# Kernel tuning notes

Measured on AMD Instinct MI355X. Metric: run time of the kernel, lower is better.

## Reference

```python
import jax, jax.numpy as jnp
import numpy as np

NUM_MOE = 64
DIM = 64


def setup_inputs() -> dict:
    key = jax.random.key(0)
    k1, k2 = jax.random.split(key)
    x = jax.random.normal(k1, (32, 8192, DIM), dtype=jnp.float32)
    # nn.Linear(dim, num_moe, bias=False): weight shape [num_moe, dim]
    W = jax.random.normal(k2, (NUM_MOE, DIM), dtype=jnp.float32) * (1.0 / np.sqrt(DIM))
    return {"x": x, "W": W, "topk": 2}


def reference(x, W, topk):
    # logits = x @ W.T  -> [B, S, E]
    logits = jnp.einsum("bsd,ed->bse", x, W)
    probs = jax.nn.softmax(logits, axis=-1)
    # top-k selection over experts
    _, topk_idx = jax.lax.top_k(probs, topk)  # [B, S, k]
    # scatter: keep top-k probs, fill rest with -inf. Since the scattered
    # values are exactly probs at those indices, a mask + where is identical
    # to full_like(-inf).scatter_(idx, vals).
    mask = jnp.sum(jax.nn.one_hot(topk_idx, NUM_MOE, dtype=jnp.bool_), axis=-2) > 0  # [B,S,E]
    topk_probs = jnp.where(mask, probs, -jnp.inf)
    # renormalize with a second softmax (non-selected experts -> 0)
    return jax.nn.softmax(topk_probs, axis=-1)
```

## Files before the change

### kernel.cpp

```cpp
#include <hip/hip_runtime.h>
#include <math.h>

#define NUM_MOE 64
#define DIM 64
#define CH 16
#define TOK 64
#define NW 4
#define ET 8

typedef float f32x2 __attribute__((ext_vector_type(2)));
typedef float f32x4 __attribute__((ext_vector_type(4)));
typedef float f32x8 __attribute__((ext_vector_type(8)));

__global__ __launch_bounds__(256)
void moe_router_kernel(const float* __restrict__ x,
                       const float* __restrict__ W,
                       float* __restrict__ out,
                       int ntok) {
    __shared__ f32x4 xs[TOK * CH];
    __shared__ float pm1[NW][TOK], pm2[NW][TOK], pz[NW][TOK];
    __shared__ int   pi1[NW][TOK], pi2[NW][TOK];

    const int tid    = threadIdx.x;
    const long tbase = (long)blockIdx.x * TOK;

    {
        const f32x4* __restrict__ g4 = reinterpret_cast<const f32x4*>(x) + tbase * CH;
        #pragma unroll
        for (int j = 0; j < 4; ++j) {
            const int G  = tid + j * 256;
            const int tk = G >> 4;
            const int c  = G & 15;
            const int Gc = (tbase + tk < ntok) ? G : (G & 15);
            xs[tk * CH + (c ^ (tk & 7))] = g4[Gc];
        }
    }

    {
        f32x4* __restrict__ ob = reinterpret_cast<f32x4*>(out) + tbase * CH;
        const f32x4 z4 = {0.0f, 0.0f, 0.0f, 0.0f};
        #pragma unroll
        for (int j = 0; j < 4; ++j) {
            const int F = tid + j * 256;
            if (tbase + (F >> 4) < ntok) ob[F] = z4;
        }
    }
    __syncthreads();

    const int lane = tid & 63;
    const int wid  = __builtin_amdgcn_readfirstlane(tid >> 6);
    const f32x8* __restrict__ Wg8 =
        reinterpret_cast<const f32x8*>(W) + (size_t)wid * 16 * (DIM / 8);

    float m1 = -INFINITY, m2 = -INFINITY, Zp = 0.0f;
    int   i1 = 0, i2 = 0;

    #pragma unroll
    for (int p = 0; p < 2; ++p) {
        f32x2 acc[ET];
        #pragma unroll
        for (int e = 0; e < ET; ++e) acc[e] = (f32x2){0.0f, 0.0f};

        #pragma unroll
        for (int k8 = 0; k8 < 8; ++k8) {
            const f32x4 xk0 = xs[lane * CH + ((2 * k8) ^ (lane & 7))];
            const f32x4 xk1 = xs[lane * CH + ((2 * k8 + 1) ^ (lane & 7))];
            const f32x2 xa = {xk0.x, xk0.y};
            const f32x2 xb = {xk0.z, xk0.w};
            const f32x2 xc = {xk1.x, xk1.y};
            const f32x2 xd = {xk1.z, xk1.w};
            #pragma unroll
            for (int e = 0; e < ET; ++e) {
                const f32x8 w8 = Wg8[(p * ET + e) * (DIM / 8) + k8];
                const f32x2 wa = {w8[0], w8[1]};
                const f32x2 wb = {w8[2], w8[3]};
                const f32x2 wc = {w8[4], w8[5]};
                const f32x2 wd = {w8[6], w8[7]};
                acc[e] = __builtin_elementwise_fma(xa, wa, acc[e]);
                acc[e] = __builtin_elementwise_fma(xb, wb, acc[e]);
                acc[e] = __builtin_elementwise_fma(xc, wc, acc[e]);
                acc[e] = __builtin_elementwise_fma(xd, wd, acc[e]);
            }
        }
        #pragma unroll
        for (int e = 0; e < ET; ++e) {
            const float v  = acc[e].x + acc[e].y;
            const int   ge = wid * 16 + p * ET + e;
            Zp += __expf(v);
            const bool b1 = v > m1;
            const bool b2 = v > m2;
            i2 = b1 ? i1 : (b2 ? ge : i2);
            m2 = b1 ? m1 : (b2 ? v : m2);
            i1 = b1 ? ge : i1;
            m1 = b1 ? v  : m1;
        }
    }

    pm1[wid][lane] = m1;  pm2[wid][lane] = m2;  pz[wid][lane] = Zp;
    pi1[wid][lane] = i1;  pi2[wid][lane] = i2;
    __syncthreads();

    if (tid < 64) {
        const int tk = tid;
        float M1 = pm1[0][tk], M2 = pm2[0][tk], Z = pz[0][tk];
        int   I1 = pi1[0][tk], I2 = pi2[0][tk];
        #pragma unroll
        for (int w = 1; w < NW; ++w) {
            const float b1 = pm1[w][tk], b2 = pm2[w][tk];
            const int   j1 = pi1[w][tk], j2 = pi2[w][tk];
            Z += pz[w][tk];
            const bool rep = b1 > M1;
            const float nm2 = rep ? ((b2 > M1) ? b2 : M1) : ((b1 > M2) ? b1 : M2);
            const int   ni2 = rep ? ((b2 > M1) ? j2 : I1) : ((b1 > M2) ? j1 : I2);
            M1 = rep ? b1 : M1;
            I1 = rep ? j1 : I1;
            M2 = nm2;  I2 = ni2;
        }

        const float E1  = __expf(M1), E2 = __expf(M2);
        const float d12 = (E1 - E2) / Z;
        const float w1  = 1.0f / (1.0f + __expf(-d12));
        const float w2  = 1.0f - w1;

        if (tbase + tk < ntok) {
            float* __restrict__ orow = out + (tbase + tk) * DIM;
            orow[I1] = w1;
            orow[I2] = w2;
        }
    }
}

extern "C" void kernel_launch(void* const* d_in, const int* in_sizes, int n_in,
                              void* d_out, int out_size, void* d_ws, size_t ws_size,
                              hipStream_t stream) {
    const float* x = (const float*)d_in[0];
    const float* W = (const float*)d_in[1];
    float* out = (float*)d_out;
    int ntok = in_sizes[0] / DIM;

    int blocks = (ntok + TOK - 1) / TOK;
    moe_router_kernel<<<blocks, 256, 0, stream>>>(x, W, out, ntok);
}
```

Before: 42.22 us.

## Process four token tiles per block with double-buffered register prefetch

Each block now loops over four 64-token tiles, loading the next tile's x into registers while computing the current one, then storing it to a second shared-memory buffer. The final top-2 reduction is rotated across waves, and the partial results are packed into fewer shared arrays. The aim is to hide global load latency and amortise per-block setup. The trade-off is fewer blocks, less occupancy-based latency hiding, and zero-fill stores that are all issued and waited on up front.

```diff
diff --git a/kernel.cpp b/kernel.cpp
--- a/kernel.cpp
+++ b/kernel.cpp
@@ -7,6 +7,7 @@
 #define TOK 64
 #define NW 4
 #define ET 8
+#define NT 4
 
 typedef float f32x2 __attribute__((ext_vector_type(2)));
 typedef float f32x4 __attribute__((ext_vector_type(4)));
@@ -17,115 +18,148 @@
                        const float* __restrict__ W,
                        float* __restrict__ out,
                        int ntok) {
-    __shared__ f32x4 xs[TOK * CH];
-    __shared__ float pm1[NW][TOK], pm2[NW][TOK], pz[NW][TOK];
-    __shared__ int   pi1[NW][TOK], pi2[NW][TOK];
-
-    const int tid    = threadIdx.x;
-    const long tbase = (long)blockIdx.x * TOK;
-
-    {
-        const f32x4* __restrict__ g4 = reinterpret_cast<const f32x4*>(x) + tbase * CH;
-        #pragma unroll
-        for (int j = 0; j < 4; ++j) {
-            const int G  = tid + j * 256;
-            const int tk = G >> 4;
-            const int c  = G & 15;
-            const int Gc = (tbase + tk < ntok) ? G : (G & 15);
-            xs[tk * CH + (c ^ (tk & 7))] = g4[Gc];
-        }
-    }
-
-    {
-        f32x4* __restrict__ ob = reinterpret_cast<f32x4*>(out) + tbase * CH;
-        const f32x4 z4 = {0.0f, 0.0f, 0.0f, 0.0f};
-        #pragma unroll
-        for (int j = 0; j < 4; ++j) {
-            const int F = tid + j * 256;
-            if (tbase + (F >> 4) < ntok) ob[F] = z4;
-        }
-    }
-    __syncthreads();
-
+    __shared__ f32x4 xs[2][TOK * CH];
+    __shared__ f32x2 pmm[2][NW][TOK];
+    __shared__ float pzz[2][NW][TOK];
+    __shared__ int   pii[2][NW][TOK];
+    const int tid  = threadIdx.x;
     const int lane = tid & 63;
     const int wid  = __builtin_amdgcn_readfirstlane(tid >> 6);
+    const long tile0 = (long)blockIdx.x * NT;
+
+    const f32x4* __restrict__ g4 = reinterpret_cast<const f32x4*>(x);
     const f32x8* __restrict__ Wg8 =
         reinterpret_cast<const f32x8*>(W) + (size_t)wid * 16 * (DIM / 8);
 
-    float m1 = -INFINITY, m2 = -INFINITY, Zp = 0.0f;
-    int   i1 = 0, i2 = 0;
+    f32x4 st[4];
+    {
+        const long tb = tile0 * TOK;
+        #pragma unroll
+        for (int j = 0; j < 4; ++j) {
+            const int G = tid + j * 256;
+            const long tk = tb + (G >> 4);
+            st[j] = g4[(tk < ntok) ? (tb * CH + G) : 0];
+        }
+    }
+    {
+        f32x4* __restrict__ ob = reinterpret_cast<f32x4*>(out) + tile0 * TOK * CH;
+        const f32x4 z4 = {0.0f, 0.0f, 0.0f, 0.0f};
+        #pragma unroll
+        for (int jj = 0; jj < 4 * NT; ++jj) {
+            const int F = tid + jj * 256;
+            if (tile0 * TOK + (F >> 4) < ntok) ob[F] = z4;
+        }
+    }
+    #pragma unroll
+    for (int j = 0; j < 4; ++j) {
+        const int G  = tid + j * 256;
+        const int tk = G >> 4, c = G & 15;
+        xs[0][tk * CH + (c ^ (tk & 7))] = st[j];
+    }
+    asm volatile("s_waitcnt vmcnt(0)" ::: "memory");
+    __syncthreads();
 
-    #pragma unroll
-    for (int p = 0; p < 2; ++p) {
-        f32x2 acc[ET];
-        #pragma unroll
-        for (int e = 0; e < ET; ++e) acc[e] = (f32x2){0.0f, 0.0f};
+    for (int it = 0; it < NT; ++it) {
+        const int  c  = it & 1;
+        const long tb = (tile0 + it) * TOK;
+        const bool have_next = (it + 1 < NT);
+
+        if (have_next) {
+            const long tbn = (tile0 + it + 1) * TOK;
+            #pragma unroll
+            for (int j = 0; j < 4; ++j) {
+                const int G = tid + j * 256;
+                const long tk = tbn + (G >> 4);
+                st[j] = g4[(tk < ntok) ? (tbn * CH + G) : 0];
+            }
+        }
+
+        float m1 = -INFINITY, m2 = -INFINITY, Zp = 0.0f;
+        int   i1 = 0, i2 = 0;
 
         #pragma unroll
-        for (int k8 = 0; k8 < 8; ++k8) {
-            const f32x4 xk0 = xs[lane * CH + ((2 * k8) ^ (lane & 7))];
-            const f32x4 xk1 = xs[lane * CH + ((2 * k8 + 1) ^ (lane & 7))];
-            const f32x2 xa = {xk0.x, xk0.y};
-            const f32x2 xb = {xk0.z, xk0.w};
-            const f32x2 xc = {xk1.x, xk1.y};
-            const f32x2 xd = {xk1.z, xk1.w};
+        for (int p = 0; p < 2; ++p) {
+            f32x2 acc[ET];
+            #pragma unroll
+            for (int e = 0; e < ET; ++e) acc[e] = (f32x2){0.0f, 0.0f};
+
+            #pragma unroll
+            for (int k8 = 0; k8 < 8; ++k8) {
+                const f32x4 xk0 = xs[c][lane * CH + ((2 * k8) ^ (lane & 7))];
+                const f32x4 xk1 = xs[c][lane * CH + ((2 * k8 + 1) ^ (lane & 7))];
+                const f32x2 xa = {xk0.x, xk0.y};
+                const f32x2 xb = {xk0.z, xk0.w};
+                const f32x2 xc = {xk1.x, xk1.y};
+                const f32x2 xd = {xk1.z, xk1.w};
+                #pragma unroll
+                for (int e = 0; e < ET; ++e) {
+                    const f32x8 w8 = Wg8[(p * ET + e) * (DIM / 8) + k8];
+                    const f32x2 wa = {w8[0], w8[1]};
+                    const f32x2 wb = {w8[2], w8[3]};
+                    const f32x2 wc = {w8[4], w8[5]};
+                    const f32x2 wd = {w8[6], w8[7]};
+                    acc[e] = __builtin_elementwise_fma(xa, wa, acc[e]);
+                    acc[e] = __builtin_elementwise_fma(xb, wb, acc[e]);
+                    acc[e] = __builtin_elementwise_fma(xc, wc, acc[e]);
+                    acc[e] = __builtin_elementwise_fma(xd, wd, acc[e]);
+                }
+            }
+            if (p == 0 && have_next) {
+                #pragma unroll
+                for (int j = 0; j < 4; ++j) {
+                    const int G  = tid + j * 256;
+                    const int tk = G >> 4, cc = G & 15;
+                    xs[c ^ 1][tk * CH + (cc ^ (tk & 7))] = st[j];
+                }
+            }
             #pragma unroll
             for (int e = 0; e < ET; ++e) {
-                const f32x8 w8 = Wg8[(p * ET + e) * (DIM / 8) + k8];
-                const f32x2 wa = {w8[0], w8[1]};
-                const f32x2 wb = {w8[2], w8[3]};
-                const f32x2 wc = {w8[4], w8[5]};
-                const f32x2 wd = {w8[6], w8[7]};
-                acc[e] = __builtin_elementwise_fma(xa, wa, acc[e]);
-                acc[e] = __builtin_elementwise_fma(xb, wb, acc[e]);
-                acc[e] = __builtin_elementwise_fma(xc, wc, acc[e]);
-                acc[e] = __builtin_elementwise_fma(xd, wd, acc[e]);
+                const float v  = acc[e].x + acc[e].y;
+                const int   ge = wid * 16 + p * ET + e;
+                Zp += __expf(v);
+                const bool b1 = v > m1;
+                const bool b2 = v > m2;
+                i2 = b1 ? i1 : (b2 ? ge : i2);
+                m2 = b1 ? m1 : (b2 ? v : m2);
+                i1 = b1 ? ge : i1;
+                m1 = b1 ? v  : m1;
             }
         }
-        #pragma unroll
-        for (int e = 0; e < ET; ++e) {
-            const float v  = acc[e].x + acc[e].y;
-            const int   ge = wid * 16 + p * ET + e;
-            Zp += __expf(v);
-            const bool b1 = v > m1;
-            const bool b2 = v > m2;
-            i2 = b1 ? i1 : (b2 ? ge : i2);
-            m2 = b1 ? m1 : (b2 ? v : m2);
-            i1 = b1 ? ge : i1;
-            m1 = b1 ? v  : m1;
-        }
-    }
 
-    pm1[wid][lane] = m1;  pm2[wid][lane] = m2;  pz[wid][lane] = Zp;
-    pi1[wid][lane] = i1;  pi2[wid][lane] = i2;
-    __syncthreads();
+        pmm[c][wid][lane] = (f32x2){m1, m2};
+        pzz[c][wid][lane] = Zp;
+        pii[c][wid][lane] = i1 | (i2 << 8);
+        __syncthreads();
 
-    if (tid < 64) {
-        const int tk = tid;
-        float M1 = pm1[0][tk], M2 = pm2[0][tk], Z = pz[0][tk];
-        int   I1 = pi1[0][tk], I2 = pi2[0][tk];
-        #pragma unroll
-        for (int w = 1; w < NW; ++w) {
-            const float b1 = pm1[w][tk], b2 = pm2[w][tk];
-            const int   j1 = pi1[w][tk], j2 = pi2[w][tk];
-            Z += pz[w][tk];
-            const bool rep = b1 > M1;
-            const float nm2 = rep ? ((b2 > M1) ? b2 : M1) : ((b1 > M2) ? b1 : M2);
-            const int   ni2 = rep ? ((b2 > M1) ? j2 : I1) : ((b1 > M2) ? j1 : I2);
-            M1 = rep ? b1 : M1;
-            I1 = rep ? j1 : I1;
-            M2 = nm2;  I2 = ni2;
-        }
-
-        const float E1  = __expf(M1), E2 = __expf(M2);
-        const float d12 = (E1 - E2) / Z;
-        const float w1  = 1.0f / (1.0f + __expf(-d12));
-        const float w2  = 1.0f - w1;
-
-        if (tbase + tk < ntok) {
-            float* __restrict__ orow = out + (tbase + tk) * DIM;
-            orow[I1] = w1;
-            orow[I2] = w2;
+        if (wid == (it & (NW - 1))) {
+            const int tk = lane;
+            f32x2 mm0 = pmm[c][0][tk];
+            float M1 = mm0.x, M2 = mm0.y, Z = pzz[c][0][tk];
+            int   pk0 = pii[c][0][tk];
+            int   I1 = pk0 & 0xFF, I2 = pk0 >> 8;
+            #pragma unroll
+            for (int w = 1; w < NW; ++w) {
+                const f32x2 mmw = pmm[c][w][tk];
+                const float b1 = mmw.x, b2 = mmw.y;
+                const int   pkw = pii[c][w][tk];
+                const int   j1 = pkw & 0xFF, j2 = pkw >> 8;
+                Z += pzz[c][w][tk];
+                const bool rep = b1 > M1;
+                const float nm2 = rep ? ((b2 > M1) ? b2 : M1) : ((b1 > M2) ? b1 : M2);
+                const int   ni2 = rep ? ((b2 > M1) ? j2 : I1) : ((b1 > M2) ? j1 : I2);
+                M1 = rep ? b1 : M1;
+                I1 = rep ? j1 : I1;
+                M2 = nm2;  I2 = ni2;
+            }
+            const float E1  = __expf(M1), E2 = __expf(M2);
+            const float d12 = (E1 - E2) / Z;
+            const float w1  = 1.0f / (1.0f + __expf(-d12));
+            const float w2  = 1.0f - w1;
+            if (tb + tk < ntok) {
+                float* __restrict__ orow = out + (tb + tk) * DIM;
+                orow[I1] = w1;
+                orow[I2] = w2;
+            }
         }
     }
 }
@@ -138,6 +172,7 @@
     float* out = (float*)d_out;
     int ntok = in_sizes[0] / DIM;
 
-    int blocks = (ntok + TOK - 1) / TOK;
+    int tiles  = (ntok + TOK - 1) / TOK;
+    int blocks = (tiles + NT - 1) / NT;
     moe_router_kernel<<<blocks, 256, 0, stream>>>(x, W, out, ntok);
 }
```

After: 89.64 us. 112% more time.

## Process two tokens per lane with 128-token tiles to reuse weight loads

Applied to the files above, without the earlier changes.

Doubles the tokens per block from 64 to 128 and has each lane compute logits for two tokens, so each W vector load feeds twice as many FMAs. The shared-memory partial results are packed, with the two maxima in an f32x2 and the two indices in one int. The aim is to cut weight-load and per-block overhead per token. In exchange it raises register pressure and LDS use, and halves the block count, which may reduce occupancy and latency hiding.

```diff
diff --git a/kernel.cpp b/kernel.cpp
--- a/kernel.cpp
+++ b/kernel.cpp
@@ -4,7 +4,7 @@
 #define NUM_MOE 64
 #define DIM 64
 #define CH 16
-#define TOK 64
+#define TOK 128
 #define NW 4
 #define ET 8
 
@@ -18,16 +18,16 @@
                        float* __restrict__ out,
                        int ntok) {
     __shared__ f32x4 xs[TOK * CH];
-    __shared__ float pm1[NW][TOK], pm2[NW][TOK], pz[NW][TOK];
-    __shared__ int   pi1[NW][TOK], pi2[NW][TOK];
-
+    __shared__ f32x2 pmm[NW][TOK];
+    __shared__ float pzz[NW][TOK];
+    __shared__ int   pii[NW][TOK];
     const int tid    = threadIdx.x;
     const long tbase = (long)blockIdx.x * TOK;
 
     {
         const f32x4* __restrict__ g4 = reinterpret_cast<const f32x4*>(x) + tbase * CH;
         #pragma unroll
-        for (int j = 0; j < 4; ++j) {
+        for (int j = 0; j < 8; ++j) {
             const int G  = tid + j * 256;
             const int tk = G >> 4;
             const int c  = G & 15;
@@ -35,12 +35,11 @@
             xs[tk * CH + (c ^ (tk & 7))] = g4[Gc];
         }
     }
-
     {
         f32x4* __restrict__ ob = reinterpret_cast<f32x4*>(out) + tbase * CH;
         const f32x4 z4 = {0.0f, 0.0f, 0.0f, 0.0f};
         #pragma unroll
-        for (int j = 0; j < 4; ++j) {
+        for (int j = 0; j < 8; ++j) {
             const int F = tid + j * 256;
             if (tbase + (F >> 4) < ntok) ob[F] = z4;
         }
@@ -52,23 +51,30 @@
     const f32x8* __restrict__ Wg8 =
         reinterpret_cast<const f32x8*>(W) + (size_t)wid * 16 * (DIM / 8);
 
-    float m1 = -INFINITY, m2 = -INFINITY, Zp = 0.0f;
-    int   i1 = 0, i2 = 0;
+    float m1A = -INFINITY, m2A = -INFINITY, ZpA = 0.0f;
+    float m1B = -INFINITY, m2B = -INFINITY, ZpB = 0.0f;
+    int   i1A = 0, i2A = 0, i1B = 0, i2B = 0;
 
     #pragma unroll
     for (int p = 0; p < 2; ++p) {
-        f32x2 acc[ET];
+        f32x2 accA[ET], accB[ET];
         #pragma unroll
-        for (int e = 0; e < ET; ++e) acc[e] = (f32x2){0.0f, 0.0f};
+        for (int e = 0; e < ET; ++e) {
+            accA[e] = (f32x2){0.0f, 0.0f};
+            accB[e] = (f32x2){0.0f, 0.0f};
+        }
 
         #pragma unroll
         for (int k8 = 0; k8 < 8; ++k8) {
-            const f32x4 xk0 = xs[lane * CH + ((2 * k8) ^ (lane & 7))];
-            const f32x4 xk1 = xs[lane * CH + ((2 * k8 + 1) ^ (lane & 7))];
-            const f32x2 xa = {xk0.x, xk0.y};
-            const f32x2 xb = {xk0.z, xk0.w};
-            const f32x2 xc = {xk1.x, xk1.y};
-            const f32x2 xd = {xk1.z, xk1.w};
+            const int sw0 = (2 * k8) ^ (lane & 7), sw1 = (2 * k8 + 1) ^ (lane & 7);
+            const f32x4 a0 = xs[lane * CH + sw0];
+            const f32x4 a1 = xs[lane * CH + sw1];
+            const f32x4 b0 = xs[(lane + 64) * CH + sw0];
+            const f32x4 b1 = xs[(lane + 64) * CH + sw1];
+            const f32x2 xaA = {a0.x, a0.y}, xbA = {a0.z, a0.w};
+            const f32x2 xcA = {a1.x, a1.y}, xdA = {a1.z, a1.w};
+            const f32x2 xaB = {b0.x, b0.y}, xbB = {b0.z, b0.w};
+            const f32x2 xcB = {b1.x, b1.y}, xdB = {b1.z, b1.w};
             #pragma unroll
             for (int e = 0; e < ET; ++e) {
                 const f32x8 w8 = Wg8[(p * ET + e) * (DIM / 8) + k8];
@@ -76,39 +82,63 @@
                 const f32x2 wb = {w8[2], w8[3]};
                 const f32x2 wc = {w8[4], w8[5]};
                 const f32x2 wd = {w8[6], w8[7]};
-                acc[e] = __builtin_elementwise_fma(xa, wa, acc[e]);
-                acc[e] = __builtin_elementwise_fma(xb, wb, acc[e]);
-                acc[e] = __builtin_elementwise_fma(xc, wc, acc[e]);
-                acc[e] = __builtin_elementwise_fma(xd, wd, acc[e]);
+                accA[e] = __builtin_elementwise_fma(xaA, wa, accA[e]);
+                accA[e] = __builtin_elementwise_fma(xbA, wb, accA[e]);
+                accA[e] = __builtin_elementwise_fma(xcA, wc, accA[e]);
+                accA[e] = __builtin_elementwise_fma(xdA, wd, accA[e]);
+                accB[e] = __builtin_elementwise_fma(xaB, wa, accB[e]);
+                accB[e] = __builtin_elementwise_fma(xbB, wb, accB[e]);
+                accB[e] = __builtin_elementwise_fma(xcB, wc, accB[e]);
+                accB[e] = __builtin_elementwise_fma(xdB, wd, accB[e]);
             }
         }
         #pragma unroll
         for (int e = 0; e < ET; ++e) {
-            const float v  = acc[e].x + acc[e].y;
-            const int   ge = wid * 16 + p * ET + e;
-            Zp += __expf(v);
-            const bool b1 = v > m1;
-            const bool b2 = v > m2;
-            i2 = b1 ? i1 : (b2 ? ge : i2);
-            m2 = b1 ? m1 : (b2 ? v : m2);
-            i1 = b1 ? ge : i1;
-            m1 = b1 ? v  : m1;
+            const int ge = wid * 16 + p * ET + e;
+            {
+                const float v = accA[e].x + accA[e].y;
+                ZpA += __expf(v);
+                const bool b1 = v > m1A;
+                const bool b2 = v > m2A;
+                i2A = b1 ? i1A : (b2 ? ge : i2A);
+                m2A = b1 ? m1A : (b2 ? v : m2A);
+                i1A = b1 ? ge : i1A;
+                m1A = b1 ? v  : m1A;
+            }
+            {
+                const float v = accB[e].x + accB[e].y;
+                ZpB += __expf(v);
+                const bool b1 = v > m1B;
+                const bool b2 = v > m2B;
+                i2B = b1 ? i1B : (b2 ? ge : i2B);
+                m2B = b1 ? m1B : (b2 ? v : m2B);
+                i1B = b1 ? ge : i1B;
+                m1B = b1 ? v  : m1B;
+            }
         }
     }
 
-    pm1[wid][lane] = m1;  pm2[wid][lane] = m2;  pz[wid][lane] = Zp;
-    pi1[wid][lane] = i1;  pi2[wid][lane] = i2;
+    pmm[wid][lane]      = (f32x2){m1A, m2A};
+    pzz[wid][lane]      = ZpA;
+    pii[wid][lane]      = i1A | (i2A << 8);
+    pmm[wid][lane + 64] = (f32x2){m1B, m2B};
+    pzz[wid][lane + 64] = ZpB;
+    pii[wid][lane + 64] = i1B | (i2B << 8);
     __syncthreads();
 
-    if (tid < 64) {
+    if (tid < TOK) {
         const int tk = tid;
-        float M1 = pm1[0][tk], M2 = pm2[0][tk], Z = pz[0][tk];
-        int   I1 = pi1[0][tk], I2 = pi2[0][tk];
+        f32x2 mm0 = pmm[0][tk];
+        float M1 = mm0.x, M2 = mm0.y, Z = pzz[0][tk];
+        int   pk0 = pii[0][tk];
+        int   I1 = pk0 & 0xFF, I2 = pk0 >> 8;
         #pragma unroll
         for (int w = 1; w < NW; ++w) {
-            const float b1 = pm1[w][tk], b2 = pm2[w][tk];
-            const int   j1 = pi1[w][tk], j2 = pi2[w][tk];
-            Z += pz[w][tk];
+            const f32x2 mmw = pmm[w][tk];
+            const float b1 = mmw.x, b2 = mmw.y;
+            const int   pkw = pii[w][tk];
+            const int   j1 = pkw & 0xFF, j2 = pkw >> 8;
+            Z += pzz[w][tk];
             const bool rep = b1 > M1;
             const float nm2 = rep ? ((b2 > M1) ? b2 : M1) : ((b1 > M2) ? b1 : M2);
             const int   ni2 = rep ? ((b2 > M1) ? j2 : I1) : ((b1 > M2) ? j1 : I2);
```

Result: slower. 46.25 us (+9.5%).
